# Kernel tuning notes

Measured on AMD Instinct MI355X. Metric: run time of the kernel, lower is better.

Reference implementation:

```python
import jax, jax.numpy as jnp
import numpy as np

N = 8192
D_IN = 256
D_OUT = 256


def setup_inputs() -> dict:
    key = jax.random.key(0)
    k1, k2, k3 = jax.random.split(key, 3)
    input = jax.random.normal(k1, (N, D_IN), dtype=jnp.float32)
    adjacencyMatrix = jax.random.uniform(k2, (N, N), dtype=jnp.float32)
    W = jax.random.normal(k3, (D_OUT, D_IN), dtype=jnp.float32) * (1.0 / np.sqrt(D_IN))
    return {"input": input, "adjacencyMatrix": adjacencyMatrix, "W": W}


def reference(input, adjacencyMatrix, W):
    # degree^{-1/2} from row sums
    d_inv_sqrt = jnp.sum(adjacencyMatrix, axis=1) ** -0.5  # [N]
    # D^{-1/2} A D^{-1/2} as row/column scaling (same math as diag matmuls)
    A_norm = adjacencyMatrix * d_inv_sqrt[:, None] * d_inv_sqrt[None, :]  # [N, N]
    # A_norm @ X @ W^T (nn.Linear without bias)
    h = A_norm @ input            # [N, D_IN]
    return h @ W.T                # [N, D_OUT]
```

## Files before the change

### kernel.cpp

```cpp
#include <hip/hip_runtime.h>
#include <stdint.h>

#define NROWS 8192
#define KDIM  8192
#define DIN   256
#define DOUT  256

typedef __attribute__((ext_vector_type(8))) short bf16x8;
typedef __attribute__((ext_vector_type(4))) float f32x4;

__device__ __forceinline__ unsigned short f2bf(float f) {
    union { float f; unsigned u; } v; v.f = f;
    unsigned r = v.u + 0x7FFFu + ((v.u >> 16) & 1u);
    return (unsigned short)(r >> 16);
}

__device__ __forceinline__ void async_load16(const void* g, void* l) {
    __builtin_amdgcn_global_load_lds(
        (__attribute__((address_space(1))) void*)(void*)g,
        (__attribute__((address_space(3))) void*)l, 16, 0, 0);
}

__global__ __launch_bounds__(256) void k_rowsum(const float* __restrict__ A,
                                                float* __restrict__ dis) {
    const int wave = threadIdx.x >> 6, lane = threadIdx.x & 63;
    const int row = (blockIdx.x << 2) + wave;
    const float4* rp = (const float4*)(A + (size_t)row * KDIM);
    float s0 = 0.f, s1 = 0.f;
    #pragma unroll
    for (int it = 0; it < 32; it += 2) {
        float4 v0 = rp[(it + 0) * 64 + lane];
        float4 v1 = rp[(it + 1) * 64 + lane];
        s0 += (v0.x + v0.y) + (v0.z + v0.w);
        s1 += (v1.x + v1.y) + (v1.z + v1.w);
    }
    float s = s0 + s1;
    #pragma unroll
    for (int off = 32; off > 0; off >>= 1) s += __shfl_down(s, off, 64);
    if (lane == 0) dis[row] = rsqrtf(s);
}

__global__ __launch_bounds__(256, 2) void k_xw(const float* __restrict__ X,
                                               const float* __restrict__ W,
                                               const float* __restrict__ dis,
                                               unsigned short* __restrict__ Zst) {
    __shared__ short sX[64 * 72];
    __shared__ short sW[256 * 72];
    __shared__ float disS[64];
    const int tid = threadIdx.x;
    const int w = tid >> 6, lane = tid & 63, lm = lane & 15, lq = lane >> 4;
    const int j0 = blockIdx.x * 64;
    if (tid < 64) disS[tid] = dis[j0 + tid];
    f32x4 acc[4][4] = {};

    for (int s = 0; s < 4; ++s) {
        const int k0 = s * 64;
        #pragma unroll
        for (int i = 0; i < 4; ++i) {
            int e = tid + i * 256;
            int row = e >> 4, c4 = e & 15;
            float4 v = *(const float4*)(X + (size_t)(j0 + row) * DIN + k0 + c4 * 4);
            short4 b; b.x = (short)f2bf(v.x); b.y = (short)f2bf(v.y);
            b.z = (short)f2bf(v.z); b.w = (short)f2bf(v.w);
            *(short4*)&sX[row * 72 + c4 * 4] = b;
        }
        #pragma unroll
        for (int i = 0; i < 16; ++i) {
            int e = tid + i * 256;
            int row = e >> 4, c4 = e & 15;
            float4 v = *(const float4*)(W + (size_t)row * DIN + k0 + c4 * 4);
            short4 b; b.x = (short)f2bf(v.x); b.y = (short)f2bf(v.y);
            b.z = (short)f2bf(v.z); b.w = (short)f2bf(v.w);
            *(short4*)&sW[row * 72 + c4 * 4] = b;
        }
        __syncthreads();
        #pragma unroll
        for (int kk = 0; kk < 2; ++kk) {
            const int koff = kk * 32 + lq * 8;
            bf16x8 a[4], b[4];
            #pragma unroll
            for (int mt = 0; mt < 4; ++mt)
                a[mt] = *(const bf16x8*)&sX[(mt * 16 + lm) * 72 + koff];
            #pragma unroll
            for (int nt = 0; nt < 4; ++nt)
                b[nt] = *(const bf16x8*)&sW[(w * 64 + nt * 16 + lm) * 72 + koff];
            #pragma unroll
            for (int mt = 0; mt < 4; ++mt)
                #pragma unroll
                for (int nt = 0; nt < 4; ++nt)
                    acc[mt][nt] = __builtin_amdgcn_mfma_f32_16x16x32_bf16(
                        a[mt], b[nt], acc[mt][nt], 0, 0, 0);
        }
        __syncthreads();
    }

    #pragma unroll
    for (int mt = 0; mt < 4; ++mt)
        #pragma unroll
        for (int nt = 0; nt < 4; ++nt)
            #pragma unroll
            for (int r = 0; r < 4; ++r) {
                int jl = mt * 16 + lq * 4 + r;
                int n  = w * 64 + nt * 16 + lm;
                float v = acc[mt][nt][r] * disS[jl];
                sW[n * 72 + jl] = (short)f2bf(v);
            }
    __syncthreads();
    #pragma unroll
    for (int it = 0; it < 8; ++it) {
        int e = tid + it * 256;
        int n = e >> 3, ch = e & 7;
        bf16x8 val = *(const bf16x8*)&sW[n * 72 + ch * 8];
        *(bf16x8*)(Zst + (size_t)n * NROWS + j0 + ch * 8) = val;
    }
}

__global__ __launch_bounds__(256, 2) void k_gemm(const float* __restrict__ A,
                                                 const unsigned short* __restrict__ Zst,
                                                 const float* __restrict__ dis,
                                                 float* __restrict__ out) {
    __shared__ short sA[64 * 72];
    __shared__ short sB[256 * 64];
    __shared__ float disS[64];
    const int tid = threadIdx.x;
    const int w = tid >> 6, lane = tid & 63, lm = lane & 15, lq = lane >> 4;
    const int m0 = blockIdx.x * 64;
    const int split = blockIdx.y;
    const int kbase = split * 2048;
    if (tid < 64) disS[tid] = dis[m0 + tid];
    f32x4 acc[4][4] = {};
    short* sBw = &sB[w * 4096];
    const int arow = tid >> 4, ac4 = tid & 15;
    const int swz = (lane & 7) ^ (lane >> 3);
    const unsigned short* gB =
        Zst + (size_t)(w * 64 + (lane >> 3)) * KDIM + kbase + swz * 8;

    for (int s = 0; s < 32; ++s) {
        const int k0 = kbase + s * 64;
        #pragma unroll
        for (int i = 0; i < 8; ++i)
            async_load16(gB + s * 64 + (size_t)i * 8 * KDIM, &sBw[i * 512]);
        #pragma unroll
        for (int i = 0; i < 4; ++i) {
            int row = arow + i * 16;
            float4 v = *(const float4*)(A + (size_t)(m0 + row) * KDIM + k0 + ac4 * 4);
            short4 b; b.x = (short)f2bf(v.x); b.y = (short)f2bf(v.y);
            b.z = (short)f2bf(v.z); b.w = (short)f2bf(v.w);
            *(short4*)&sA[row * 72 + ac4 * 4] = b;
        }
        __syncthreads();
        #pragma unroll
        for (int kk = 0; kk < 2; ++kk) {
            const int koff = kk * 32 + lq * 8;
            const int cb = kk * 4 + lq;
            const int scb = cb ^ (lm & 7);
            bf16x8 a[4], b[4];
            #pragma unroll
            for (int mt = 0; mt < 4; ++mt)
                a[mt] = *(const bf16x8*)&sA[(mt * 16 + lm) * 72 + koff];
            #pragma unroll
            for (int nt = 0; nt < 4; ++nt)
                b[nt] = *(const bf16x8*)&sBw[(nt * 16 + lm) * 64 + scb * 8];
            #pragma unroll
            for (int mt = 0; mt < 4; ++mt)
                #pragma unroll
                for (int nt = 0; nt < 4; ++nt)
                    acc[mt][nt] = __builtin_amdgcn_mfma_f32_16x16x32_bf16(
                        a[mt], b[nt], acc[mt][nt], 0, 0, 0);
        }
        __syncthreads();
    }

    #pragma unroll
    for (int mt = 0; mt < 4; ++mt)
        #pragma unroll
        for (int nt = 0; nt < 4; ++nt) {
            int col = w * 64 + nt * 16 + lm;
            #pragma unroll
            for (int r = 0; r < 4; ++r) {
                int rl = mt * 16 + lq * 4 + r;
                atomicAdd(out + (size_t)(m0 + rl) * DOUT + col,
                          acc[mt][nt][r] * disS[rl]);
            }
        }
}

extern "C" void kernel_launch(void* const* d_in, const int* in_sizes, int n_in,
                              void* d_out, int out_size, void* d_ws, size_t ws_size,
                              hipStream_t stream) {
    const float* X = (const float*)d_in[0];
    const float* A = (const float*)d_in[1];
    const float* W = (const float*)d_in[2];
    float* out = (float*)d_out;
    char* ws = (char*)d_ws;
    float* dis = (float*)ws;
    unsigned short* Zst = (unsigned short*)(ws + 32768);

    k_rowsum<<<NROWS / 4, 256, 0, stream>>>(A, dis);
    k_xw<<<NROWS / 64, 256, 0, stream>>>(X, W, dis, Zst);
    hipMemsetAsync(d_out, 0, (size_t)out_size * sizeof(float), stream);
    k_gemm<<<dim3(NROWS / 64, 4), 256, 0, stream>>>(A, Zst, dis, out);
}
```

Before: 457.6 us.

## Merge rowsum with X·W^T, split scaling pass, replace atomics with partial-sum reduce

Runs the row-sum of A and the unscaled X·W^T product in one launch so the two independent stages can overlap, then applies the degree scaling and the bf16 conversion in a separate elementwise kernel. The split-K GEMM now writes per-split partial outputs that a final reduce kernel sums, replacing the memset and the float atomics. This adds an fp32 intermediate, an extra 32 MB of partial buffers and two more launches. If the workspace is smaller than required, nothing runs at all.

```diff
diff --git a/kernel.cpp b/kernel.cpp
--- a/kernel.cpp
+++ b/kernel.cpp
@@ -21,36 +21,37 @@
         (__attribute__((address_space(3))) void*)l, 16, 0, 0);
 }
 
-__global__ __launch_bounds__(256) void k_rowsum(const float* __restrict__ A,
-                                                float* __restrict__ dis) {
-    const int wave = threadIdx.x >> 6, lane = threadIdx.x & 63;
-    const int row = (blockIdx.x << 2) + wave;
-    const float4* rp = (const float4*)(A + (size_t)row * KDIM);
-    float s0 = 0.f, s1 = 0.f;
-    #pragma unroll
-    for (int it = 0; it < 32; it += 2) {
-        float4 v0 = rp[(it + 0) * 64 + lane];
-        float4 v1 = rp[(it + 1) * 64 + lane];
-        s0 += (v0.x + v0.y) + (v0.z + v0.w);
-        s1 += (v1.x + v1.y) + (v1.z + v1.w);
-    }
-    float s = s0 + s1;
-    #pragma unroll
-    for (int off = 32; off > 0; off >>= 1) s += __shfl_down(s, off, 64);
-    if (lane == 0) dis[row] = rsqrtf(s);
-}
-
-__global__ __launch_bounds__(256, 2) void k_xw(const float* __restrict__ X,
-                                               const float* __restrict__ W,
-                                               const float* __restrict__ dis,
-                                               unsigned short* __restrict__ Zst) {
+__global__ void k_rowsum_y(const float* __restrict__ A,
+                           const float* __restrict__ X,
+                           const float* __restrict__ W,
+                           float* __restrict__ dis,
+                           float* __restrict__ Yt) {
     __shared__ short sX[64 * 72];
     __shared__ short sW[256 * 72];
-    __shared__ float disS[64];
     const int tid = threadIdx.x;
+    const int bid = blockIdx.x;
+
+    if (bid < 2048) {
+        const int wave = tid >> 6, lane = tid & 63;
+        const int row = (bid << 2) + wave;
+        const float4* rp = (const float4*)(A + (size_t)row * KDIM);
+        float s0 = 0.f, s1 = 0.f;
+        #pragma unroll
+        for (int it = 0; it < 32; it += 2) {
+            float4 v0 = rp[(it + 0) * 64 + lane];
+            float4 v1 = rp[(it + 1) * 64 + lane];
+            s0 += (v0.x + v0.y) + (v0.z + v0.w);
+            s1 += (v1.x + v1.y) + (v1.z + v1.w);
+        }
+        float s = s0 + s1;
+        #pragma unroll
+        for (int off = 32; off > 0; off >>= 1) s += __shfl_down(s, off, 64);
+        if (lane == 0) dis[row] = rsqrtf(s);
+        return;
+    }
+
     const int w = tid >> 6, lane = tid & 63, lm = lane & 15, lq = lane >> 4;
-    const int j0 = blockIdx.x * 64;
-    if (tid < 64) disS[tid] = dis[j0 + tid];
+    const int j0 = (bid - 2048) * 64;
     f32x4 acc[4][4] = {};
 
     for (int s = 0; s < 4; ++s) {
@@ -97,28 +98,32 @@
     #pragma unroll
     for (int mt = 0; mt < 4; ++mt)
         #pragma unroll
-        for (int nt = 0; nt < 4; ++nt)
-            #pragma unroll
-            for (int r = 0; r < 4; ++r) {
-                int jl = mt * 16 + lq * 4 + r;
-                int n  = w * 64 + nt * 16 + lm;
-                float v = acc[mt][nt][r] * disS[jl];
-                sW[n * 72 + jl] = (short)f2bf(v);
-            }
-    __syncthreads();
-    #pragma unroll
-    for (int it = 0; it < 8; ++it) {
-        int e = tid + it * 256;
-        int n = e >> 3, ch = e & 7;
-        bf16x8 val = *(const bf16x8*)&sW[n * 72 + ch * 8];
-        *(bf16x8*)(Zst + (size_t)n * NROWS + j0 + ch * 8) = val;
-    }
+        for (int nt = 0; nt < 4; ++nt) {
+            int n = w * 64 + nt * 16 + lm;
+            int j = j0 + mt * 16 + lq * 4;
+            *(float4*)&Yt[(size_t)n * NROWS + j] = (float4){acc[mt][nt][0], acc[mt][nt][1],
+                                                            acc[mt][nt][2], acc[mt][nt][3]};
+        }
+}
+
+__global__ __launch_bounds__(256) void k_scale_cvt(const float* __restrict__ Yt,
+                                                   const float* __restrict__ dis,
+                                                   unsigned short* __restrict__ Zst) {
+    const size_t idx = (size_t)blockIdx.x * 256 + threadIdx.x;
+    const size_t j4 = idx & (NROWS / 4 - 1);
+    const size_t n = idx >> 11;
+    float4 y = *(const float4*)&Yt[n * NROWS + j4 * 4];
+    float4 d = *(const float4*)&dis[j4 * 4];
+    short4 b;
+    b.x = (short)f2bf(y.x * d.x); b.y = (short)f2bf(y.y * d.y);
+    b.z = (short)f2bf(y.z * d.z); b.w = (short)f2bf(y.w * d.w);
+    *(short4*)&Zst[n * NROWS + j4 * 4] = b;
 }
 
 __global__ __launch_bounds__(256, 2) void k_gemm(const float* __restrict__ A,
                                                  const unsigned short* __restrict__ Zst,
                                                  const float* __restrict__ dis,
-                                                 float* __restrict__ out) {
+                                                 float* __restrict__ part) {
     __shared__ short sA[64 * 72];
     __shared__ short sB[256 * 64];
     __shared__ float disS[64];
@@ -179,10 +184,23 @@
             #pragma unroll
             for (int r = 0; r < 4; ++r) {
                 int rl = mt * 16 + lq * 4 + r;
-                atomicAdd(out + (size_t)(m0 + rl) * DOUT + col,
-                          acc[mt][nt][r] * disS[rl]);
+                part[(size_t)split * (NROWS * DOUT) + (size_t)(m0 + rl) * DOUT + col] =
+                    acc[mt][nt][r] * disS[rl];
             }
         }
+}
+
+__global__ __launch_bounds__(256) void k_reduce(const float4* __restrict__ p,
+                                                float4* __restrict__ out) {
+    const size_t i = (size_t)blockIdx.x * 256 + threadIdx.x;
+    const size_t stride = (size_t)NROWS * DOUT / 4;
+    float4 a = p[i], b = p[i + stride], c = p[i + 2 * stride], d = p[i + 3 * stride];
+    float4 r;
+    r.x = (a.x + b.x) + (c.x + d.x);
+    r.y = (a.y + b.y) + (c.y + d.y);
+    r.z = (a.z + b.z) + (c.z + d.z);
+    r.w = (a.w + b.w) + (c.w + d.w);
+    out[i] = r;
 }
 
 extern "C" void kernel_launch(void* const* d_in, const int* in_sizes, int n_in,
@@ -195,9 +213,15 @@
     char* ws = (char*)d_ws;
     float* dis = (float*)ws;
     unsigned short* Zst = (unsigned short*)(ws + 32768);
-
-    k_rowsum<<<NROWS / 4, 256, 0, stream>>>(A, dis);
-    k_xw<<<NROWS / 64, 256, 0, stream>>>(X, W, dis, Zst);
-    hipMemsetAsync(d_out, 0, (size_t)out_size * sizeof(float), stream);
-    k_gemm<<<dim3(NROWS / 64, 4), 256, 0, stream>>>(A, Zst, dis, out);
-}
+    float* Yt = (float*)(ws + 32768 + (4ull << 20));
+    float* part = (float*)(ws + 32768 + (12ull << 20));
+    const size_t need = 32768 + (12ull << 20) + 4ull * NROWS * DOUT * sizeof(float);
+
+    if (ws_size >= need) {
+        k_rowsum_y<<<2048 + NROWS / 64, 256, 0, stream>>>(A, X, W, dis, Yt);
+        k_scale_cvt<<<(NROWS * DOUT / 4) / 256, 256, 0, stream>>>(Yt, dis, Zst);
+        k_gemm<<<dim3(NROWS / 64, 4), 256, 0, stream>>>(A, Zst, dis, part);
+        k_reduce<<<(NROWS * DOUT / 4) / 256, 256, 0, stream>>>((const float4*)part,
+                                                               (float4*)out);
+    }
+}
```

Measured after the change: 472.2 us. 3.2% more time.
